# Optimization experiments

Measured on AMD Instinct MI355X. Metric: run time of the kernel, lower is better.

The kernel has to match this reference:

```python
import jax, jax.numpy as jnp
import numpy as np

N, E, G = 8192, 65536, 64
DIMS = [(74, 2048), (2048, 1024), (1024, 512), (512, 512)]
EDGE_DIM = 21


def setup_inputs() -> dict:
    key = jax.random.key(0)
    ks = jax.random.split(key, 64)
    x = jax.random.uniform(ks[0], (N, 10), jnp.float32)
    x = x.at[:, 0].set(jax.random.randint(ks[1], (N,), 1, 119).astype(jnp.float32))
    x = x.at[:, 9].set(jax.random.randint(ks[2], (N,), 0, 2).astype(jnp.float32))
    edge_index = jax.random.randint(ks[3], (2, E), 0, N, dtype=jnp.int32)
    edge_attr = jax.random.uniform(ks[4], (E, 4), jnp.float32)
    edge_attr = edge_attr.at[:, 0].set(jax.random.randint(ks[5], (E,), 1, 22).astype(jnp.float32))
    edge_attr = edge_attr.at[:, 2].set(jax.random.randint(ks[6], (E,), 0, 2).astype(jnp.float32))
    edge_attr = edge_attr.at[:, 3].set(jax.random.randint(ks[7], (E,), 0, 2).astype(jnp.float32))
    batch = jnp.sort(jax.random.randint(ks[8], (N,), 0, G, dtype=jnp.int32))
    atom_emb = (jax.random.normal(ks[9], (119, 64), jnp.float32) * 0.1).at[0].set(0.0)
    bond_emb = (jax.random.normal(ks[10], (22, 16), jnp.float32) * 0.1).at[0].set(0.0)
    bool_emb = (jax.random.normal(ks[11], (3, 2), jnp.float32) * 0.1).at[2].set(0.0)
    inp = dict(x=x, edge_attr=edge_attr, atom_emb=atom_emb, bond_emb=bond_emb,
               bool_emb=bool_emb, edge_index=edge_index, batch=batch)
    ki = 12
    for li, (din, dout) in enumerate(DIMS, start=1):
        s = 1.0 / np.sqrt(din)
        inp[f"Wl{li}"] = jax.random.normal(ks[ki], (din, dout), jnp.float32) * s; ki += 1
        inp[f"bl{li}"] = jnp.zeros((dout,), jnp.float32)
        inp[f"Wr{li}"] = jax.random.normal(ks[ki], (din, dout), jnp.float32) * s; ki += 1
        inp[f"br{li}"] = jnp.zeros((dout,), jnp.float32)
        inp[f"We{li}"] = jax.random.normal(ks[ki], (EDGE_DIM, dout), jnp.float32) * (1.0 / np.sqrt(EDGE_DIM)); ki += 1
        inp[f"att{li}"] = jax.random.normal(ks[ki], (dout,), jnp.float32) * (1.0 / np.sqrt(dout)); ki += 1
        inp[f"b{li}"] = jnp.zeros((dout,), jnp.float32)
    return inp


def _gatv2(h, src, tgt, ea, Wl, bl, Wr, br, We, att, b):
    # PyG GATv2Conv, heads=1, negative_slope=0.2 (self-loops already appended)
    n = h.shape[0]
    xl = h @ Wl + bl                           # source transform  [N, C]
    xr = h @ Wr + br                           # target transform  [N, C]
    m = xl[src] + xr[tgt] + ea @ We            # per-edge message  [E', C]
    a = jax.nn.leaky_relu(m, 0.2) @ att        # attention logits  [E']
    amax = jax.ops.segment_max(a, tgt, num_segments=n)
    ex = jnp.exp(a - amax[tgt])                # edge softmax over incoming edges
    denom = jax.ops.segment_sum(ex, tgt, num_segments=n)
    alpha = ex / denom[tgt]
    return jax.ops.segment_sum(alpha[:, None] * xl[src], tgt, num_segments=n) + b


def _forward(x, edge_attr, atom_emb, bond_emb, bool_emb, params, edge_index, batch):
    n = x.shape[0]
    # feature encoding: [atom_emb(64) | 8 float feats | bool_emb(2)] -> 74
    h = jnp.concatenate([atom_emb[x[:, 0].astype(jnp.int32)], x[:, 1:9],
                         bool_emb[x[:, 9].astype(jnp.int32)]], axis=1)
    # edge encoding: [bond_emb(16) | 1 float | bool_emb(2) | bool_emb(2)] -> 21
    ea = jnp.concatenate([bond_emb[edge_attr[:, 0].astype(jnp.int32)], edge_attr[:, 1:2],
                          bool_emb[edge_attr[:, 2].astype(jnp.int32)],
                          bool_emb[edge_attr[:, 3].astype(jnp.int32)]], axis=1)
    src, tgt = edge_index[0], edge_index[1]
    # add_self_loops with fill_value='mean': self-loop attr = mean of incoming edge attrs
    cnt = jax.ops.segment_sum(jnp.ones(src.shape, h.dtype), tgt, num_segments=n)
    loop_attr = jax.ops.segment_sum(ea, tgt, num_segments=n) / jnp.maximum(cnt, 1.0)[:, None]
    loop = jnp.arange(n, dtype=src.dtype)
    src = jnp.concatenate([src, loop])
    tgt = jnp.concatenate([tgt, loop])
    ea = jnp.concatenate([ea, loop_attr], axis=0)
    for p in params:  # 4 GATv2 layers + ReLU (dropout = identity in eval)
        h = jax.nn.relu(_gatv2(h, src, tgt, ea, *p))
    gcnt = jax.ops.segment_sum(jnp.ones(batch.shape, h.dtype), batch, num_segments=G)
    return jax.ops.segment_sum(h, batch, num_segments=G) / jnp.maximum(gcnt, 1.0)[:, None]


def reference(x, edge_attr, atom_emb, bond_emb, bool_emb,
              Wl1, bl1, Wr1, br1, We1, att1, b1,
              Wl2, bl2, Wr2, br2, We2, att2, b2,
              Wl3, bl3, Wr3, br3, We3, att3, b3,
              Wl4, bl4, Wr4, br4, We4, att4, b4,
              edge_index, batch):
    params = [(Wl1, bl1, Wr1, br1, We1, att1, b1),
              (Wl2, bl2, Wr2, br2, We2, att2, b2),
              (Wl3, bl3, Wr3, br3, We3, att3, b3),
              (Wl4, bl4, Wr4, br4, We4, att4, b4)]
    return _forward(x, edge_attr, atom_emb, bond_emb, bool_emb, params, edge_index, batch)
```

## Files before the change

kernel.cpp:

```cpp
#include <hip/hip_runtime.h>
#include <hip/hip_bf16.h>

#define N_NODES 8192
#define N_EDGES 65536
#define EP (N_EDGES + N_NODES)
#define N_GROUPS 64
#define DEGCAP 64
#define EDGE_B 4

typedef _Float16 f16_t;
typedef f16_t  f16x8  __attribute__((ext_vector_type(8)));
typedef f16_t  h2     __attribute__((ext_vector_type(2)));
typedef f16_t  h4     __attribute__((ext_vector_type(4)));
typedef float  f32x4  __attribute__((ext_vector_type(4)));
typedef unsigned u32x2 __attribute__((ext_vector_type(2)));

__device__ __forceinline__ float lrelu(float v){ return v > 0.f ? v : 0.2f*v; }

__device__ __forceinline__ void gload_lds16(const void* g, void* l){
  typedef __attribute__((address_space(1))) const void gvoid_t;
  typedef __attribute__((address_space(3))) void lvoid_t;
  __builtin_amdgcn_global_load_lds((gvoid_t*)g, (lvoid_t*)l, 16, 0, 0);
}

__device__ __forceinline__ unsigned pkh2(float a, float b){
  union{h2 h; unsigned u;} c; c.h[0] = (f16_t)a; c.h[1] = (f16_t)b; return c.u;
}
__device__ __forceinline__ h2 as_h2(unsigned u){ union{unsigned x; h2 h;} c; c.x = u; return c.h; }
__device__ __forceinline__ unsigned pkh(f16_t a, f16_t b){
  unsigned short ua = *(unsigned short*)&a, ub = *(unsigned short*)&b;
  return (unsigned)ua | ((unsigned)ub << 16);
}

#if __has_builtin(__builtin_amdgcn_fdot2)
#define FDOT2(a,b,c) __builtin_amdgcn_fdot2((a),(b),(c),false)
#else
#define FDOT2(a,b,c) ((c) + (float)(a)[0]*(float)(b)[0] + (float)(a)[1]*(float)(b)[1])
#endif

__global__ void k_encode_nodes(const float* __restrict__ x, const float* __restrict__ atom_emb,
                               const float* __restrict__ bool_emb, float* __restrict__ h){
  int idx = blockIdx.x*blockDim.x + threadIdx.x;
  if (idx >= N_NODES*74) return;
  int n = idx / 74, c = idx % 74;
  float v;
  if (c < 64)      { int ai = (int)x[n*10+0]; v = atom_emb[ai*64 + c]; }
  else if (c < 72) { v = x[n*10 + 1 + (c-64)]; }
  else             { int bi = (int)x[n*10+9]; v = bool_emb[bi*2 + (c-72)]; }
  h[n*74 + c] = v;
}

__global__ void k_deg(const int* __restrict__ ei, int* __restrict__ deg){
  int e = blockIdx.x*blockDim.x + threadIdx.x;
  if (e >= N_EDGES) return;
  atomicAdd(&deg[ei[N_EDGES + e]], 1);
}

__global__ __launch_bounds__(1024) void k_scan(const int* __restrict__ deg, int* __restrict__ rowptr){
  __shared__ int buf[1024];
  int t = threadIdx.x;
  int loc[8]; int s = 0;
  #pragma unroll
  for (int i=0;i<8;++i){ loc[i]=s; s += deg[t*8+i] + 1; }
  buf[t] = s; __syncthreads();
  for (int off=1; off<1024; off<<=1){
    int v = (t>=off) ? buf[t-off] : 0; __syncthreads();
    buf[t] += v; __syncthreads();
  }
  int base = buf[t] - s;
  #pragma unroll
  for (int i=0;i<8;++i) rowptr[t*8+i] = base + loc[i];
  if (t==1023) rowptr[8192] = buf[1023];
}

__global__ void k_fill(const int* __restrict__ ei, const int* __restrict__ rowptr,
                       int* __restrict__ fillpos, int* __restrict__ csr_src,
                       int* __restrict__ posE){
  int e = blockIdx.x*blockDim.x + threadIdx.x;
  if (e >= EP) return;
  int s, tg;
  if (e < N_EDGES){ s = ei[e]; tg = ei[N_EDGES+e]; }
  else            { s = tg = e - N_EDGES; }
  int pos = rowptr[tg] + atomicAdd(&fillpos[tg], 1);
  csr_src[pos] = s; posE[e] = pos;
}

__global__ void k_encode_edges(const float* __restrict__ edge_attr, const float* __restrict__ bond_emb,
                               const float* __restrict__ bool_emb, const int* __restrict__ posE,
                               unsigned* __restrict__ ea_pk){
  int e = blockIdx.x*blockDim.x + threadIdx.x;
  if (e >= N_EDGES) return;
  float a0 = edge_attr[e*4+0], a1 = edge_attr[e*4+1];
  float a2 = edge_attr[e*4+2], a3 = edge_attr[e*4+3];
  int bi = (int)a0, b2 = (int)a2, b3 = (int)a3;
  int pos = posE[e];
  float v[22];
  #pragma unroll
  for (int j=0;j<16;++j) v[j] = bond_emb[bi*16+j];
  v[16] = a1;
  v[17] = bool_emb[b2*2+0]; v[18] = bool_emb[b2*2+1];
  v[19] = bool_emb[b3*2+0]; v[20] = bool_emb[b3*2+1];
  v[21] = 0.f;
  #pragma unroll
  for (int j=0;j<11;++j) ea_pk[(size_t)pos*12 + j] = pkh2(v[2*j], v[2*j+1]);
  ea_pk[(size_t)pos*12 + 11] = 0u;
}

__global__ void k_loopsum(const float* __restrict__ edge_attr, const float* __restrict__ bond_emb,
                          const float* __restrict__ bool_emb, const int* __restrict__ ei,
                          float* __restrict__ loopsum){
  int e = blockIdx.x*blockDim.x + threadIdx.x;
  if (e >= N_EDGES) return;
  float a0 = edge_attr[e*4+0], a1 = edge_attr[e*4+1];
  float a2 = edge_attr[e*4+2], a3 = edge_attr[e*4+3];
  int bi = (int)a0, b2 = (int)a2, b3 = (int)a3;
  int tg = ei[N_EDGES + e];
  float v[21];
  #pragma unroll
  for (int j=0;j<16;++j) v[j] = bond_emb[bi*16+j];
  v[16] = a1;
  v[17] = bool_emb[b2*2+0]; v[18] = bool_emb[b2*2+1];
  v[19] = bool_emb[b3*2+0]; v[20] = bool_emb[b3*2+1];
  #pragma unroll
  for (int j=0;j<21;++j) atomicAdd(&loopsum[tg*21+j], v[j]);
}

__global__ void k_loop_attr(const float* __restrict__ loopsum, const int* __restrict__ deg,
                            const int* __restrict__ posE, unsigned* __restrict__ ea_pk){
  int n = blockIdx.x*blockDim.x + threadIdx.x;
  if (n >= N_NODES) return;
  float c = (float)deg[n]; if (c < 1.f) c = 1.f;
  float inv = 1.f / c;
  int pos = posE[N_EDGES + n];
  float v[22];
  #pragma unroll
  for (int j=0;j<21;++j) v[j] = loopsum[n*21+j] * inv;
  v[21] = 0.f;
  #pragma unroll
  for (int j=0;j<11;++j) ea_pk[(size_t)pos*12 + j] = pkh2(v[2*j], v[2*j+1]);
  ea_pk[(size_t)pos*12 + 11] = 0u;
}

__global__ void k_goff(const int* __restrict__ batch, int* __restrict__ goff){
  int n = blockIdx.x*blockDim.x + threadIdx.x;
  if (n >= N_NODES) return;
  int b = batch[n];
  if (n == 0){ for (int g=0; g<=b; ++g) goff[g] = 0; }
  else { int bp = batch[n-1]; for (int g=bp+1; g<=b; ++g) goff[g] = n; }
  if (n == N_NODES-1){ for (int g=b+1; g<=N_GROUPS; ++g) goff[g] = N_NODES; }
}

__global__ void k_splitA(const float* __restrict__ A, f16_t* __restrict__ Ah,
                         f16_t* __restrict__ Al, int K, int Kp){
  int idx = blockIdx.x*blockDim.x + threadIdx.x;
  if (idx >= N_NODES*Kp) return;
  int k = idx % Kp;
  int n = idx / Kp;
  float v = (k < K) ? A[(size_t)n*K + k] : 0.f;
  f16_t hi = (f16_t)v;
  f16_t lo = (f16_t)(v - (float)hi);
  Ah[idx] = hi; Al[idx] = lo;
}

__global__ void k_splitW2(const float* __restrict__ Wl, const float* __restrict__ Wr,
                          f16_t* __restrict__ W2, int K, int Kp, int Nc){
  int idx = blockIdx.x*blockDim.x + threadIdx.x;
  if (idx >= 2*Nc*Kp) return;
  int k = idx % Kp;
  int n = idx / Kp;
  const float* W = (n < Nc) ? Wl : Wr;
  int nn = (n < Nc) ? n : n - Nc;
  float v = (k < K) ? W[(size_t)k*Nc + nn] : 0.f;
  W2[idx] = (f16_t)v;
}

__global__ void k_packWe(const float* __restrict__ We, unsigned* __restrict__ We_pk, int C){
  int c = blockIdx.x*blockDim.x + threadIdx.x;
  if (c >= C) return;
  #pragma unroll
  for (int j=0;j<10;++j)
    We_pk[(size_t)j*C + c] = pkh2(We[(size_t)(2*j)*C + c], We[(size_t)(2*j+1)*C + c]);
  We_pk[(size_t)10*C + c] = pkh2(We[(size_t)20*C + c], 0.f);
}

#define BM 128
#define BN 128
#define BK 64
__global__ __launch_bounds__(256) void k_gemm2_mfma(
    const f16_t* __restrict__ Ah, const f16_t* __restrict__ Al,
    const f16_t* __restrict__ W2,
    const float* __restrict__ bl, const float* __restrict__ br,
    f16_t* __restrict__ XLh, float* __restrict__ XR,
    int Kp, int Chalf)
{
  __shared__ __align__(16) f16_t sA[BM*BK];
  __shared__ __align__(16) f16_t sB[BN*BK];
  int t = threadIdx.x;
  int lane = t & 63;
  int w = t >> 6;
  int wr = w >> 1, wc = w & 1;
  int bm = blockIdx.y * BM, bn = blockIdx.x * BN;

  f32x4 acc[4][4] = {};

  int srow = t >> 3;
  int scol = (t & 7) * 8;

  for (int seg = 0; seg < 2; ++seg){
    const f16_t* As = seg ? Al : Ah;
    for (int k0 = 0; k0 < Kp; k0 += BK){
      #pragma unroll
      for (int i = 0; i < 4; ++i){
        int row = srow + i*32;
        gload_lds16(As + (size_t)(bm + row)*Kp + k0 + scol, (char*)sA + (t + i*256)*16);
        gload_lds16(W2 + (size_t)(bn + row)*Kp + k0 + scol, (char*)sB + (t + i*256)*16);
      }
      __syncthreads();
      #pragma unroll
      for (int kk = 0; kk < BK; kk += 32){
        f16x8 af[4], bfr[4];
        int ko = kk + (lane >> 4)*8;
        #pragma unroll
        for (int m=0;m<4;++m)
          af[m] = *(const f16x8*)&sA[(wr*64 + m*16 + (lane&15))*BK + ko];
        #pragma unroll
        for (int n=0;n<4;++n)
          bfr[n] = *(const f16x8*)&sB[(wc*64 + n*16 + (lane&15))*BK + ko];
        #pragma unroll
        for (int m=0;m<4;++m)
          #pragma unroll
          for (int n=0;n<4;++n)
            acc[m][n] = __builtin_amdgcn_mfma_f32_16x16x32_f16(af[m], bfr[n], acc[m][n], 0, 0, 0);
      }
      __syncthreads();
    }
  }

  bool left = (bn < Chalf);
  int cadj = left ? 0 : Chalf;
  const float* bias = left ? bl : br;
  int r0 = bm + wr*64 + ((lane>>4)<<2);
  int c0 = bn + wc*64 + (lane&15);
  #pragma unroll
  for (int n=0;n<4;++n){
    int col = c0 + n*16 - cadj;
    float bv = bias[col];
    #pragma unroll
    for (int m=0;m<4;++m){
      #pragma unroll
      for (int j=0;j<4;++j){
        size_t idx = (size_t)(r0 + m*16 + j)*Chalf + col;
        float v = acc[m][n][j] + bv;
        if (left) XLh[idx] = (f16_t)v;
        else      XR[idx]  = v;
      }
    }
  }
}

__global__ __launch_bounds__(256) void k_edge_fused(
    const f16_t* __restrict__ XLh,
    const float* __restrict__ XR,
    const unsigned* __restrict__ ea_pk, const unsigned* __restrict__ We_pk,
    const float* __restrict__ att, const float* __restrict__ bias,
    const int* __restrict__ rowptr, const int* __restrict__ csr_src,
    f16_t* __restrict__ AhN, f16_t* __restrict__ AlN,
    float* __restrict__ houtF, int C)
{
  __shared__ float sPart[4][DEGCAP];
  __shared__ float sAl[DEGCAP];
  __shared__ int   sSrc[DEGCAP];
  int t = threadIdx.x;
  int lane = t & 63, q = t >> 6;
  int n = blockIdx.x;
  int p0 = rowptr[n];
  int deg = rowptr[n+1] - p0;
  if (deg > DEGCAP) deg = DEGCAP;
  int p0s = __builtin_amdgcn_readfirstlane(p0);

  if (q == 0 && lane < deg) sSrc[lane] = csr_src[p0 + lane];
  __syncthreads();

  float lpart = 0.f;
  for (int g = 0; g < deg; g += EDGE_B){
    unsigned earr[EDGE_B][11];
    int sidx[EDGE_B];
    #pragma unroll
    for (int i=0;i<EDGE_B;++i){
      int qq = (g+i < deg) ? (g+i) : 0;
      sidx[i] = sSrc[qq];
      const unsigned* ep = ea_pk + (size_t)(p0s+qq)*12;
      #pragma unroll
      for (int j=0;j<11;++j) earr[i][j] = ep[j];
    }
    float acc[EDGE_B] = {0.f,0.f,0.f,0.f};
    for (int c0 = q*128; c0 < C; c0 += 512){
      int c = c0 + 2*lane;
      u32x2 wpk[11];
      #pragma unroll
      for (int j=0;j<11;++j) wpk[j] = *(const u32x2*)&We_pk[(size_t)j*C + c];
      float2 xr2 = *(const float2*)&XR[(size_t)n*C + c];
      float2 at2 = *(const float2*)&att[c];
      #pragma unroll
      for (int i=0;i<EDGE_B;++i){
        if (g+i < deg){
          h2 xl2 = as_h2(*(const unsigned*)(XLh + (size_t)sidx[i]*C + c));
          float m0 = (float)xl2[0] + xr2.x;
          float m1 = (float)xl2[1] + xr2.y;
          #pragma unroll
          for (int j=0;j<11;++j){
            h2 e = as_h2(earr[i][j]);
            m0 = FDOT2(e, as_h2(wpk[j][0]), m0);
            m1 = FDOT2(e, as_h2(wpk[j][1]), m1);
          }
          acc[i] += lrelu(m0)*at2.x + lrelu(m1)*at2.y;
        }
      }
    }
    #pragma unroll
    for (int i=0;i<EDGE_B;++i){
      if (g+i < deg){
        float v = acc[i];
        #pragma unroll
        for (int off=32; off; off>>=1) v += __shfl_xor(v, off);
        if (lane == g+i) lpart = v;
      }
    }
  }

  sPart[q][lane] = lpart;
  __syncthreads();
  if (q == 0){
    float tot = (lane < deg) ? (sPart[0][lane] + sPart[1][lane] +
                                sPart[2][lane] + sPart[3][lane]) : -1e30f;
    float mx = tot;
    #pragma unroll
    for (int off=32; off; off>>=1) mx = fmaxf(mx, __shfl_xor(mx, off));
    float ex = (lane < deg) ? __expf(tot - mx) : 0.f;
    float sm = ex;
    #pragma unroll
    for (int off=32; off; off>>=1) sm += __shfl_xor(sm, off);
    sAl[lane] = ex / sm;
  }
  __syncthreads();

  int cbase = q*(C>>2), cend = cbase + (C>>2);
  for (int c0 = cbase + 4*lane; c0 < cend; c0 += 256){
    float a0 = bias[c0], a1 = bias[c0+1], a2 = bias[c0+2], a3 = bias[c0+3];
    for (int p = 0; p < deg; ++p){
      float al = sAl[p];
      int s = sSrc[p];
      h4 hh = *(const h4*)(XLh + (size_t)s*C + c0);
      a0 += al * (float)hh[0];
      a1 += al * (float)hh[1];
      a2 += al * (float)hh[2];
      a3 += al * (float)hh[3];
    }
    float r0 = fmaxf(a0, 0.f), r1 = fmaxf(a1, 0.f);
    float r2 = fmaxf(a2, 0.f), r3 = fmaxf(a3, 0.f);
    if (houtF){
      f32x4 rv = {r0, r1, r2, r3};
      *(f32x4*)&houtF[(size_t)n*C + c0] = rv;
    } else {
      f16_t h0 = (f16_t)r0, h1 = (f16_t)r1, h2v = (f16_t)r2, h3 = (f16_t)r3;
      f16_t l0 = (f16_t)(r0 - (float)h0), l1 = (f16_t)(r1 - (float)h1);
      f16_t l2 = (f16_t)(r2 - (float)h2v), l3 = (f16_t)(r3 - (float)h3);
      u32x2 wh = {pkh(h0, h1), pkh(h2v, h3)};
      u32x2 wl = {pkh(l0, l1), pkh(l2, l3)};
      *(u32x2*)&AhN[(size_t)n*C + c0] = wh;
      *(u32x2*)&AlN[(size_t)n*C + c0] = wl;
    }
  }
}

__global__ void k_pool(const float* __restrict__ h, const int* __restrict__ goff,
                       float* __restrict__ out){
  int g = blockIdx.x >> 1;
  int c = ((blockIdx.x & 1) * 256) + threadIdx.x;
  int n0 = goff[g], n1 = goff[g+1];
  float s = 0.f;
  for (int n=n0;n<n1;++n) s += h[(size_t)n*512 + c];
  float cf = (float)(n1-n0); if (cf < 1.f) cf = 1.f;
  out[g*512 + c] = s / cf;
}

extern "C" void kernel_launch(void* const* d_in, const int* in_sizes, int n_in,
                              void* d_out, int out_size, void* d_ws, size_t ws_size,
                              hipStream_t stream) {
  (void)in_sizes; (void)n_in; (void)out_size; (void)ws_size;
  const float* x         = (const float*)d_in[0];
  const float* edge_attr = (const float*)d_in[1];
  const float* atom_emb  = (const float*)d_in[2];
  const float* bond_emb  = (const float*)d_in[3];
  const float* bool_emb  = (const float*)d_in[4];
  const int*   ei        = (const int*)d_in[5];
  const int*   batch     = (const int*)d_in[6];

  struct Layer { const float *Wl,*bl,*Wr,*br,*We,*att,*b; int Cin,Cout,Kp; };
  const int dims[5] = {74, 2048, 1024, 512, 512};
  const int kpad[4] = {128, 2048, 1024, 512};
  Layer L[4];
  for (int i=0;i<4;++i){
    const int o = 7 + i*7;
    L[i] = { (const float*)d_in[o+0], (const float*)d_in[o+1], (const float*)d_in[o+2],
             (const float*)d_in[o+3], (const float*)d_in[o+4], (const float*)d_in[o+5],
             (const float*)d_in[o+6], dims[i], dims[i+1], kpad[i] };
  }

  char* ws = (char*)d_ws;
  size_t off = 0;
  auto alloc = [&](size_t bytes)->void*{ void* p = ws + off; off += (bytes + 255) & ~(size_t)255; return p; };
  f16_t* p0Ah = (f16_t*)alloc((size_t)N_NODES*1024*2);
  f16_t* p0Al = (f16_t*)alloc((size_t)N_NODES*1024*2);
  f16_t* p1Ah = (f16_t*)alloc((size_t)N_NODES*2048*2);
  f16_t* p1Al = (f16_t*)alloc((size_t)N_NODES*2048*2);
  f16_t* XLh  = (f16_t*)alloc((size_t)N_NODES*2048*2);
  float* XR   = (float*)alloc((size_t)N_NODES*2048*4);
  float* hfin = (float*)alloc((size_t)N_NODES*512*4);
  float* h0   = (float*)alloc((size_t)N_NODES*74*4);
  f16_t* W2b  = (f16_t*)alloc((size_t)2*1024*2048*2);
  unsigned* We_pk = (unsigned*)alloc((size_t)11*2048*4);
  unsigned* ea_pk = (unsigned*)alloc((size_t)EP*12*4);
  float* loopsum = (float*)alloc((size_t)N_NODES*21*4);
  int*   deg     = (int*)alloc((size_t)N_NODES*4);
  int*   rowptr  = (int*)alloc((size_t)(N_NODES+1)*4);
  int*   fillpos = (int*)alloc((size_t)N_NODES*4);
  int*   csr_src = (int*)alloc((size_t)EP*4);
  int*   posE    = (int*)alloc((size_t)EP*4);
  int*   goff    = (int*)alloc((size_t)(N_GROUPS+1)*4);

  hipMemsetAsync(loopsum, 0, (size_t)N_NODES*21*4, stream);
  hipMemsetAsync(deg,     0, (size_t)N_NODES*4, stream);
  hipMemsetAsync(fillpos, 0, (size_t)N_NODES*4, stream);

  k_encode_nodes<<<(N_NODES*74 + 255)/256, 256, 0, stream>>>(x, atom_emb, bool_emb, h0);
  k_deg<<<N_EDGES/256, 256, 0, stream>>>(ei, deg);
  k_scan<<<1, 1024, 0, stream>>>(deg, rowptr);
  k_fill<<<(EP + 255)/256, 256, 0, stream>>>(ei, rowptr, fillpos, csr_src, posE);
  k_encode_edges<<<N_EDGES/256, 256, 0, stream>>>(edge_attr, bond_emb, bool_emb, posE, ea_pk);
  k_loopsum<<<N_EDGES/256, 256, 0, stream>>>(edge_attr, bond_emb, bool_emb, ei, loopsum);
  k_loop_attr<<<(N_NODES + 255)/256, 256, 0, stream>>>(loopsum, deg, posE, ea_pk);
  k_goff<<<N_NODES/256, 256, 0, stream>>>(batch, goff);

  k_splitA<<<((size_t)N_NODES*128 + 255)/256, 256, 0, stream>>>(h0, p0Ah, p0Al, 74, 128);

  f16_t* pairAh[2] = { p0Ah, p1Ah };
  f16_t* pairAl[2] = { p0Al, p1Al };
  for (int li=0; li<4; ++li){
    int cur = li & 1, nxt = cur ^ 1;
    int C = L[li].Cout, Kp = L[li].Kp;
    dim3 ggrid(2*C/BN, N_NODES/BM);

    k_splitW2<<<((size_t)2*C*Kp + 255)/256, 256, 0, stream>>>(L[li].Wl, L[li].Wr, W2b,
                                                              L[li].Cin, Kp, C);
    k_gemm2_mfma<<<ggrid, 256, 0, stream>>>(pairAh[cur], pairAl[cur], W2b,
                                            L[li].bl, L[li].br, XLh, XR, Kp, C);

    k_packWe<<<(C + 255)/256, 256, 0, stream>>>(L[li].We, We_pk, C);

    if (li < 3)
      k_edge_fused<<<N_NODES, 256, 0, stream>>>(XLh, XR, ea_pk, We_pk, L[li].att,
                                                L[li].b, rowptr, csr_src,
                                                pairAh[nxt], pairAl[nxt],
                                                (float*)nullptr, C);
    else
      k_edge_fused<<<N_NODES, 256, 0, stream>>>(XLh, XR, ea_pk, We_pk, L[li].att,
                                                L[li].b, rowptr, csr_src,
                                                (f16_t*)nullptr, (f16_t*)nullptr,
                                                hfin, C);
  }

  k_pool<<<N_GROUPS*2, 256, 0, stream>>>(hfin, goff, (float*)d_out);
}
```

Measured before the change: 998.0 us.

## Order edge blocks by descending degree and remap GEMM blocks across XCDs

Adds a counting-sort pass that builds a permutation of nodes in descending degree order. The edge-fused kernel reads its node through this permutation so that high-degree nodes start first, which reduces tail imbalance. The GEMM also remaps its linear workgroup ID so that consecutive tiles land on the same XCD, aiming for better L2 reuse across MI355X chiplets. This costs three small extra preprocessing kernels and scatters the edge kernel's output writes.

```diff
diff --git a/kernel.cpp b/kernel.cpp
--- a/kernel.cpp
+++ b/kernel.cpp
@@ -83,6 +83,27 @@
   else            { s = tg = e - N_EDGES; }
   int pos = rowptr[tg] + atomicAdd(&fillpos[tg], 1);
   csr_src[pos] = s; posE[e] = pos;
+}
+
+__global__ void k_dhist(const int* __restrict__ rowptr, int* __restrict__ hist){
+  int n = blockIdx.x*blockDim.x + threadIdx.x;
+  if (n >= N_NODES) return;
+  int d = rowptr[n+1] - rowptr[n];
+  if (d > DEGCAP) d = DEGCAP;
+  atomicAdd(&hist[d], 1);
+}
+__global__ void k_dscan(const int* __restrict__ hist, int* __restrict__ boff){
+  if (threadIdx.x || blockIdx.x) return;
+  int acc = 0;
+  for (int d = DEGCAP; d >= 0; --d){ boff[d] = acc; acc += hist[d]; }
+}
+__global__ void k_dscatter(const int* __restrict__ rowptr, const int* __restrict__ boff,
+                           int* __restrict__ bcnt, int* __restrict__ perm){
+  int n = blockIdx.x*blockDim.x + threadIdx.x;
+  if (n >= N_NODES) return;
+  int d = rowptr[n+1] - rowptr[n];
+  if (d > DEGCAP) d = DEGCAP;
+  perm[boff[d] + atomicAdd(&bcnt[d], 1)] = n;
 }
 
 __global__ void k_encode_edges(const float* __restrict__ edge_attr, const float* __restrict__ bond_emb,
@@ -199,7 +220,14 @@
   int lane = t & 63;
   int w = t >> 6;
   int wr = w >> 1, wc = w & 1;
-  int bm = blockIdx.y * BM, bn = blockIdx.x * BN;
+
+  int lin = blockIdx.y * gridDim.x + blockIdx.x;
+  int nwg = gridDim.x * gridDim.y;
+  int qd = nwg >> 3, rm = nwg & 7;
+  int xcd = lin & 7, sub = lin >> 3;
+  int work = (xcd < rm ? xcd*(qd+1) : rm*(qd+1) + (xcd-rm)*qd) + sub;
+  int bn = (work % gridDim.x) * BN;
+  int bm = (work / gridDim.x) * BM;
 
   f32x4 acc[4][4] = {};
 
@@ -264,6 +292,7 @@
     const unsigned* __restrict__ ea_pk, const unsigned* __restrict__ We_pk,
     const float* __restrict__ att, const float* __restrict__ bias,
     const int* __restrict__ rowptr, const int* __restrict__ csr_src,
+    const int* __restrict__ perm,
     f16_t* __restrict__ AhN, f16_t* __restrict__ AlN,
     float* __restrict__ houtF, int C)
 {
@@ -272,7 +301,7 @@
   __shared__ int   sSrc[DEGCAP];
   int t = threadIdx.x;
   int lane = t & 63, q = t >> 6;
-  int n = blockIdx.x;
+  int n = perm[blockIdx.x];
   int p0 = rowptr[n];
   int deg = rowptr[n+1] - p0;
   if (deg > DEGCAP) deg = DEGCAP;
@@ -428,15 +457,24 @@
   int*   csr_src = (int*)alloc((size_t)EP*4);
   int*   posE    = (int*)alloc((size_t)EP*4);
   int*   goff    = (int*)alloc((size_t)(N_GROUPS+1)*4);
+  int*   dhist   = (int*)alloc((size_t)(DEGCAP+1)*4);
+  int*   dboff   = (int*)alloc((size_t)(DEGCAP+1)*4);
+  int*   dbcnt   = (int*)alloc((size_t)(DEGCAP+1)*4);
+  int*   perm    = (int*)alloc((size_t)N_NODES*4);
 
   hipMemsetAsync(loopsum, 0, (size_t)N_NODES*21*4, stream);
   hipMemsetAsync(deg,     0, (size_t)N_NODES*4, stream);
   hipMemsetAsync(fillpos, 0, (size_t)N_NODES*4, stream);
+  hipMemsetAsync(dhist,   0, (size_t)(DEGCAP+1)*4, stream);
+  hipMemsetAsync(dbcnt,   0, (size_t)(DEGCAP+1)*4, stream);
 
   k_encode_nodes<<<(N_NODES*74 + 255)/256, 256, 0, stream>>>(x, atom_emb, bool_emb, h0);
   k_deg<<<N_EDGES/256, 256, 0, stream>>>(ei, deg);
   k_scan<<<1, 1024, 0, stream>>>(deg, rowptr);
   k_fill<<<(EP + 255)/256, 256, 0, stream>>>(ei, rowptr, fillpos, csr_src, posE);
+  k_dhist<<<N_NODES/256, 256, 0, stream>>>(rowptr, dhist);
+  k_dscan<<<1, 64, 0, stream>>>(dhist, dboff);
+  k_dscatter<<<N_NODES/256, 256, 0, stream>>>(rowptr, dboff, dbcnt, perm);
   k_encode_edges<<<N_EDGES/256, 256, 0, stream>>>(edge_attr, bond_emb, bool_emb, posE, ea_pk);
   k_loopsum<<<N_EDGES/256, 256, 0, stream>>>(edge_attr, bond_emb, bool_emb, ei, loopsum);
   k_loop_attr<<<(N_NODES + 255)/256, 256, 0, stream>>>(loopsum, deg, posE, ea_pk);
@@ -460,12 +498,12 @@
 
     if (li < 3)
       k_edge_fused<<<N_NODES, 256, 0, stream>>>(XLh, XR, ea_pk, We_pk, L[li].att,
-                                                L[li].b, rowptr, csr_src,
+                                                L[li].b, rowptr, csr_src, perm,
                                                 pairAh[nxt], pairAl[nxt],
                                                 (float*)nullptr, C);
     else
       k_edge_fused<<<N_NODES, 256, 0, stream>>>(XLh, XR, ea_pk, We_pk, L[li].att,
-                                                L[li].b, rowptr, csr_src,
+                                                L[li].b, rowptr, csr_src, perm,
                                                 (f16_t*)nullptr, (f16_t*)nullptr,
                                                 hfin, C);
   }
```

After: 1.026 ms. 2.8% more time.
